# Optimization experiments

Hardware: AMD Instinct MI355X
Metric: run time of the kernel (lower is better)

## Reference

```python
import jax, jax.numpy as jnp
import numpy as np

DIM = 512
HEADS = 8
DIM_HEAD = 64
INNER = HEADS * DIM_HEAD  # 512
B, N = 4, 2048


def setup_inputs() -> dict:
    key = jax.random.key(0)
    k1, k2, k3, k4 = jax.random.split(key, 4)
    x = jax.random.normal(k1, (B, N, DIM), dtype=jnp.float32)
    # nn.Linear(dim, inner*3, bias=False): weight [3*inner, dim]; store transposed [dim, 3*inner]
    w_qkv = jax.random.normal(k2, (DIM, 3 * INNER), dtype=jnp.float32) / np.sqrt(DIM)
    w_out = jax.random.normal(k3, (INNER, DIM), dtype=jnp.float32) / np.sqrt(INNER)
    b_out = jax.random.normal(k4, (DIM,), dtype=jnp.float32) * 0.01
    return {"x": x, "w_qkv": w_qkv, "w_out": w_out, "b_out": b_out}


def reference(x, w_qkv, w_out, b_out):
    b, n, _ = x.shape
    scale = DIM_HEAD ** -0.5
    qkv = x @ w_qkv  # [b, n, 3*inner]
    q, k, v = jnp.split(qkv, 3, axis=-1)
    # [b, n, h, d] -> [b, h, n, d]
    reshape = lambda t: t.reshape(b, n, HEADS, DIM_HEAD).transpose(0, 2, 1, 3)
    q, k, v = reshape(q), reshape(k), reshape(v)
    dots = jnp.einsum('bhid,bhjd->bhij', q, k) * scale  # [b, h, n, n]
    attn = jax.nn.softmax(dots, axis=-1)
    out = jnp.einsum('bhij,bhjd->bhid', attn, v)  # [b, h, n, d]
    out = out.transpose(0, 2, 1, 3).reshape(b, n, INNER)
    return out @ w_out + b_out  # dropout is identity at inference
```

## Files before the change

### kernel.cpp

```cpp
#include <hip/hip_runtime.h>
#include <hip/hip_bf16.h>
#include <cstdint>

#define DEV __device__ __forceinline__

typedef __attribute__((ext_vector_type(8))) __bf16 bf16x8;
typedef __attribute__((ext_vector_type(4))) float floatx4;
typedef __attribute__((ext_vector_type(4))) short shortx4;
typedef __attribute__((ext_vector_type(8))) short shortx8;

constexpr float QSCALE = 0.18033688011112042f;

DEV unsigned short f2b(float f) {
  union { float f; unsigned u; } v; v.f = f;
  return (unsigned short)((v.u + 0x7fffu + ((v.u >> 16) & 1u)) >> 16);
}

#if defined(__has_builtin) && __has_builtin(__builtin_amdgcn_cvt_pk_bf16_f32)
DEV unsigned pk2(float a, float b) {
  typedef __attribute__((ext_vector_type(2))) __bf16 bf2;
  union { bf2 v; unsigned u; } u;
  u.v = __builtin_amdgcn_cvt_pk_bf16_f32(a, b);
  return u.u;
}
#else
DEV unsigned pk2(float a, float b) {
  return (unsigned)f2b(a) | ((unsigned)f2b(b) << 16);
}
#endif

#if defined(__has_builtin) && __has_builtin(__builtin_amdgcn_exp2f)
DEV float fexp2(float x) { return __builtin_amdgcn_exp2f(x); }
#else
DEV float fexp2(float x) { return exp2f(x); }
#endif

DEV floatx4 mfma16(bf16x8 a, bf16x8 b, floatx4 c) {
  return __builtin_amdgcn_mfma_f32_16x16x32_bf16(a, b, c, 0, 0, 0);
}

#define GLD_LDS16(gp, lp)                                                          \
  __builtin_amdgcn_global_load_lds(                                                \
      (const __attribute__((address_space(1))) void*)(gp),                         \
      (__attribute__((address_space(3))) void*)(lp), 16, 0, 0)

__global__ void prep(const float* __restrict__ x,
                     const float* __restrict__ w_qkv,
                     const float* __restrict__ w_out,
                     unsigned short* __restrict__ xb,
                     unsigned short* __restrict__ wqkvt,
                     unsigned short* __restrict__ woutt) {
  __shared__ float tile[32][33];
  if (blockIdx.x < 4096) {
    int i = blockIdx.x * 256 + threadIdx.x;
    floatx4 f = ((const floatx4*)x)[i];
    shortx4 s;
    s[0] = (short)f2b(f[0]); s[1] = (short)f2b(f[1]);
    s[2] = (short)f2b(f[2]); s[3] = (short)f2b(f[3]);
    ((shortx4*)xb)[i] = s;
    return;
  }
  int id = blockIdx.x - 4096;
  int bxr = id & 63, by = id >> 6;
  const float* in; unsigned short* out; int C, bx;
  if (bxr < 48) { in = w_qkv; out = wqkvt; C = 1536; bx = bxr; }
  else { in = w_out; out = woutt; C = 512; bx = bxr - 48; }
  const int R = 512;
  int tx = threadIdx.x & 31, ty = threadIdx.x >> 5;
  int r0 = by * 32, c0 = bx * 32;
#pragma unroll
  for (int i = 0; i < 4; i++) {
    int rr = ty + i * 8;
    tile[rr][tx] = in[(size_t)(r0 + rr) * C + c0 + tx];
  }
  __syncthreads();
#pragma unroll
  for (int i = 0; i < 4; i++) {
    int rr = ty + i * 8;
    out[(size_t)(c0 + rr) * R + r0 + tx] = f2b(tile[tx][rr]);
  }
}

__global__ __launch_bounds__(256, 3) void gemm_qkv(
    const unsigned short* __restrict__ A, const unsigned short* __restrict__ Bt,
    unsigned short* __restrict__ qf, unsigned short* __restrict__ kg,
    unsigned short* __restrict__ vf) {
  __shared__ __align__(16) unsigned short smem[17408];
  const int tid = threadIdx.x;
  const int lane = tid & 63, wid = tid >> 6;
  const int g = lane >> 4, r = lane & 15;
  const int flat = blockIdx.y * 12 + blockIdx.x;
  const int sw = (flat & 7) * 96 + (flat >> 3);
  const int bx = sw % 12, by = sw / 12;
  const int m0 = by * 128, n0 = bx * 128;
  const int wm = (wid & 1) * 64, wn = (wid >> 1) * 64;
  const int K = 512;

  floatx4 acc[4][4] = {};

  int rowA[2], kbA[2];
#pragma unroll
  for (int i = 0; i < 2; i++) {
    int c = i * 256 + tid;
    rowA[i] = c >> 2;
    kbA[i] = (c & 3) ^ ((rowA[i] >> 1) & 3);
  }

#define STAGE_G(kt, b)                                                           \
  {                                                                              \
    _Pragma("unroll") for (int i = 0; i < 2; i++) {                              \
      GLD_LDS16(A + (size_t)(m0 + rowA[i]) * K + (kt) + kbA[i] * 8,              \
                (char*)smem + (b)*8192 + i * 4096 + wid * 1024);                 \
      GLD_LDS16(Bt + (size_t)(n0 + rowA[i]) * K + (kt) + kbA[i] * 8,             \
                (char*)smem + 16384 + (b)*8192 + i * 4096 + wid * 1024);         \
    }                                                                            \
  }

  STAGE_G(0, 0)
  for (int it = 0; it < 16; it++) {
    const int buf = it & 1;
    __syncthreads();
    if (it + 1 < 16) STAGE_G((it + 1) * 32, buf ^ 1)
    const unsigned short* Xs = smem + buf * 4096;
    const unsigned short* Ws = smem + 8192 + buf * 4096;
    bf16x8 a[4], b[4];
#pragma unroll
    for (int t = 0; t < 4; t++) {
      int rw = wm + t * 16 + r;
      a[t] = *(const bf16x8*)(Xs + rw * 32 + (g ^ ((rw >> 1) & 3)) * 8);
      int rb = wn + t * 16 + r;
      b[t] = *(const bf16x8*)(Ws + rb * 32 + (g ^ ((rb >> 1) & 3)) * 8);
    }
#pragma unroll
    for (int mt = 0; mt < 4; mt++)
#pragma unroll
      for (int nt = 0; nt < 4; nt++)
        acc[mt][nt] = mfma16(a[mt], b[nt], acc[mt][nt]);
  }
#undef STAGE_G

  const int which = bx >> 2;
  if (which == 2) {
    const int tokbase = m0 + wm;
    const int bb = tokbase >> 11, vt = (tokbase & 2047) >> 6;
#pragma unroll
    for (int nt = 0; nt < 4; nt++) {
      int vcol = n0 + wn + nt * 16 + r - 1024;
      int h = vcol >> 6;
      size_t hb = (size_t)(bb * 8 + h) * 131072 + (size_t)vt * 4096 + nt * 1024 +
                  (g * 16 + r) * 8;
#pragma unroll
      for (int kc = 0; kc < 2; kc++) {
        union { unsigned u[4]; shortx8 v; } w;
        w.u[0] = pk2(acc[2 * kc][nt][0], acc[2 * kc][nt][1]);
        w.u[1] = pk2(acc[2 * kc][nt][2], acc[2 * kc][nt][3]);
        w.u[2] = pk2(acc[2 * kc + 1][nt][0], acc[2 * kc + 1][nt][1]);
        w.u[3] = pk2(acc[2 * kc + 1][nt][2], acc[2 * kc + 1][nt][3]);
        *(shortx8*)(vf + hb + kc * 512) = w.v;
      }
    }
  } else {
    const float sc = (which == 0) ? QSCALE : 1.f;
    __syncthreads();
#pragma unroll
    for (int mt = 0; mt < 4; mt++)
#pragma unroll
      for (int nt = 0; nt < 4; nt++) {
        int col = wn + nt * 16 + r;
#pragma unroll
        for (int e = 0; e < 4; e++)
          smem[(wm + mt * 16 + g * 4 + e) * 136 + col] = f2b(acc[mt][nt][e] * sc);
      }
    __syncthreads();
#pragma unroll
    for (int it = 0; it < 8; it++) {
      int c = it * 256 + tid;
      int row = c >> 4, cc = c & 15;
      shortx8 v = *(const shortx8*)(smem + row * 136 + cc * 8);
      int gq = n0 + cc * 8;
      int h = (gq >> 6) & 7, d0 = gq & 63;
      int tok = m0 + row, bb = tok >> 11, n = tok & 2047;
      if (which == 0) {
        int kc = d0 >> 5, gp = (d0 >> 3) & 3;
        *(shortx8*)(qf + (size_t)(bb * 8 + h) * 131072 + (n >> 4) * 1024 +
                    kc * 512 + (gp * 16 + (n & 15)) * 8) = v;
      } else {
        *(shortx8*)(kg + ((size_t)(bb * 8 + h) * 2048 + n) * 64 + d0) = v;
      }
    }
  }
}

__global__ __launch_bounds__(256, 2) void gemm_out(
    const unsigned short* __restrict__ A, const unsigned short* __restrict__ Bt,
    float* __restrict__ outF, const float* __restrict__ bias) {
  __shared__ __align__(16) unsigned short smem[16896];
  const int tid = threadIdx.x;
  const int lane = tid & 63, wid = tid >> 6;
  const int g = lane >> 4, r = lane & 15;
  const int m0 = blockIdx.y * 64, n0 = blockIdx.x * 128;
  const int wn = wid * 32;
  const int K = 512;

  floatx4 acc[4][2] = {};

  const int rA = tid >> 2, kA = (tid & 3) ^ ((rA >> 1) & 3);
  int rB[2], kB[2];
#pragma unroll
  for (int i = 0; i < 2; i++) {
    int c = i * 256 + tid;
    rB[i] = c >> 2;
    kB[i] = (c & 3) ^ ((rB[i] >> 1) & 3);
  }

#define STAGE_O(kt, b)                                                           \
  {                                                                              \
    GLD_LDS16(A + (size_t)(m0 + rA) * K + (kt) + kA * 8,                         \
              (char*)smem + (b)*4096 + wid * 1024);                              \
    _Pragma("unroll") for (int i = 0; i < 2; i++)                                \
        GLD_LDS16(Bt + (size_t)(n0 + rB[i]) * K + (kt) + kB[i] * 8,              \
                  (char*)smem + 8192 + (b)*8192 + i * 4096 + wid * 1024);        \
  }

  STAGE_O(0, 0)
  for (int it = 0; it < 16; it++) {
    const int buf = it & 1;
    __syncthreads();
    if (it + 1 < 16) STAGE_O((it + 1) * 32, buf ^ 1)
    const unsigned short* Xs = smem + buf * 2048;
    const unsigned short* Ws = smem + 4096 + buf * 4096;
    bf16x8 a[4], b[2];
#pragma unroll
    for (int t = 0; t < 4; t++) {
      int rw = t * 16 + r;
      a[t] = *(const bf16x8*)(Xs + rw * 32 + (g ^ ((rw >> 1) & 3)) * 8);
    }
#pragma unroll
    for (int t = 0; t < 2; t++) {
      int rb = wn + t * 16 + r;
      b[t] = *(const bf16x8*)(Ws + rb * 32 + (g ^ ((rb >> 1) & 3)) * 8);
    }
#pragma unroll
    for (int mt = 0; mt < 4; mt++)
#pragma unroll
      for (int bt = 0; bt < 2; bt++)
        acc[mt][bt] = mfma16(a[mt], b[bt], acc[mt][bt]);
  }
#undef STAGE_O

  float* ftile = (float*)smem;
  __syncthreads();
#pragma unroll
  for (int mt = 0; mt < 4; mt++)
#pragma unroll
    for (int bt = 0; bt < 2; bt++)
#pragma unroll
      for (int e = 0; e < 4; e++)
        ftile[(mt * 16 + g * 4 + e) * 132 + wn + bt * 16 + r] = acc[mt][bt][e];
  __syncthreads();
#pragma unroll
  for (int it = 0; it < 8; it++) {
    int c = it * 256 + tid;
    int lr = c >> 5, cc = c & 31;
    floatx4 v = *(const floatx4*)(ftile + lr * 132 + cc * 4);
    int col = n0 + cc * 4;
    v += *(const floatx4*)(bias + col);
    *(floatx4*)(outF + (size_t)(m0 + lr) * 512 + col) = v;
  }
}

__global__ __launch_bounds__(256, 2) void attn(
    const unsigned short* __restrict__ qf, const unsigned short* __restrict__ kg,
    const unsigned short* __restrict__ vf, unsigned short* __restrict__ ao) {
  __shared__ __align__(16) char L[65536];
  unsigned short* Ksm = (unsigned short*)L;
  const int tid = threadIdx.x, lane = tid & 63, wid = tid >> 6;
  const int g = lane >> 4, r = lane & 15, r7 = r & 7;
  const int wq = wid & 1, wk = wid >> 1;
  const int slot = blockIdx.x;
  const int bh = ((slot & 7) << 2) | ((slot >> 3) & 3);
  const int qt = slot >> 5;
  const size_t kbase = (size_t)bh * (2048 * 64);
  const size_t fbase = (size_t)bh * 131072;
  const int srow = lane >> 3;
  const int chunk = (lane & 7) ^ (srow & 7);

  const int qt0 = qt * 8 + wq * 4;
  bf16x8 bq[4][2];
#pragma unroll
  for (int nt = 0; nt < 4; nt++)
#pragma unroll
    for (int kc = 0; kc < 2; kc++)
      bq[nt][kc] = *(const bf16x8*)(qf + fbase + (size_t)(qt0 + nt) * 1024 +
                                    kc * 512 + lane * 8);

  bf16x8 vones;
#pragma unroll
  for (int i = 0; i < 8; i++) vones[i] = (__bf16)1.0f;
  const floatx4 fzero = {0.f, 0.f, 0.f, 0.f};

  floatx4 o[4][4] = {};
  floatx4 lacc[4] = {};

  const unsigned short* vbp = vf + fbase + (size_t)(wk * 2) * 4096 + lane * 8;
  const unsigned short* kgp =
      kg + kbase + (size_t)(wid * 64 + srow) * 64 + chunk * 8;

#define STAGE_K(b)                                                               \
  {                                                                              \
    _Pragma("unroll") for (int j = 0; j < 8; j++) {                              \
      GLD_LDS16(kgp + j * 512, (char*)L + (b)*32768 + wid * 8192 + j * 1024);    \
    }                                                                            \
    kgp += 16384;                                                                \
  }

  STAGE_K(0)
  for (int rnd = 0; rnd < 8; rnd++) {
    const int buf = rnd & 1;
    __syncthreads();
    if (rnd + 1 < 8) STAGE_K(buf ^ 1)
    const unsigned short* Kt = Ksm + buf * 16384 + wk * 8192;
#pragma unroll
    for (int sub = 0; sub < 2; sub++) {
      const unsigned short* Ks_ = Kt + sub * 4096;

      bf16x8 bv[4][2];
#pragma unroll
      for (int b = 0; b < 4; b++)
#pragma unroll
        for (int kc = 0; kc < 2; kc++)
          bv[b][kc] = *(const bf16x8*)(vbp + sub * 4096 + b * 1024 + kc * 512);

      floatx4 st[4][4];
      __builtin_amdgcn_s_setprio(1);
#pragma unroll
      for (int mt = 0; mt < 4; mt++) {
        bf16x8 ak0 = *(const bf16x8*)(Ks_ + (mt * 16 + r) * 64 + (g ^ r7) * 8);
        bf16x8 ak1 =
            *(const bf16x8*)(Ks_ + (mt * 16 + r) * 64 + ((4 + g) ^ r7) * 8);
#pragma unroll
        for (int nt = 0; nt < 4; nt++) {
          floatx4 t = mfma16(ak0, bq[nt][0], fzero);
          st[mt][nt] = mfma16(ak1, bq[nt][1], t);
        }
      }
      __builtin_amdgcn_s_setprio(0);

      bf16x8 ap[4][2];
#pragma unroll
      for (int a = 0; a < 4; a++) {
        float p[4][4];
#pragma unroll
        for (int mt = 0; mt < 4; mt++)
#pragma unroll
          for (int e = 0; e < 4; e++) p[mt][e] = fexp2(st[mt][a][e]);
#pragma unroll
        for (int kc = 0; kc < 2; kc++) {
          union { unsigned u[4]; bf16x8 v; } w;
          w.u[0] = pk2(p[2 * kc][0], p[2 * kc][1]);
          w.u[1] = pk2(p[2 * kc][2], p[2 * kc][3]);
          w.u[2] = pk2(p[2 * kc + 1][0], p[2 * kc + 1][1]);
          w.u[3] = pk2(p[2 * kc + 1][2], p[2 * kc + 1][3]);
          ap[a][kc] = w.v;
        }
      }

      __builtin_amdgcn_s_setprio(1);
#pragma unroll
      for (int kc = 0; kc < 2; kc++)
#pragma unroll
        for (int a = 0; a < 4; a++) {
          lacc[a] = mfma16(ap[a][kc], vones, lacc[a]);
#pragma unroll
          for (int b = 0; b < 4; b++)
            o[a][b] = mfma16(ap[a][kc], bv[b][kc], o[a][b]);
        }
      __builtin_amdgcn_s_setprio(0);
    }
    vbp += 16384;
  }
#undef STAGE_K

  float* fP = (float*)L;
  float* fL = (float*)(L + 32768);
  unsigned short* Osm = (unsigned short*)(L + 40960);
  __syncthreads();
  if (wk == 1) {
#pragma unroll
    for (int a = 0; a < 4; a++) {
      *(floatx4*)&fL[wq * 1024 + a * 256 + lane * 4] = lacc[a];
#pragma unroll
      for (int b = 0; b < 4; b++)
        *(floatx4*)&fP[wq * 4096 + (a * 4 + b) * 256 + lane * 4] = o[a][b];
    }
  }
  __syncthreads();
  if (wk == 0) {
#pragma unroll
    for (int a = 0; a < 4; a++) {
      floatx4 lt = lacc[a] + *(floatx4*)&fL[wq * 1024 + a * 256 + lane * 4];
      floatx4 il;
#pragma unroll
      for (int e = 0; e < 4; e++) il[e] = 1.f / lt[e];
#pragma unroll
      for (int b = 0; b < 4; b++) {
        floatx4 oo = o[a][b] +
                     *(floatx4*)&fP[wq * 4096 + (a * 4 + b) * 256 + lane * 4];
#pragma unroll
        for (int e = 0; e < 4; e++)
          Osm[wq * 4608 + (a * 16 + g * 4 + e) * 72 + b * 16 + r] =
              f2b(oo[e] * il[e]);
      }
    }
  }
  __syncthreads();
  const int bb = bh >> 3, h = bh & 7;
#pragma unroll
  for (int it = 0; it < 4; it++) {
    int c = it * 256 + tid;
    int row = c >> 3, cc = c & 7;
    int wqi = row >> 6, r6 = row & 63;
    shortx8 v = *(const shortx8*)(Osm + wqi * 4608 + r6 * 72 + cc * 8);
    int tok = qt * 128 + row;
    *(shortx8*)(ao + ((size_t)(bb * 2048 + tok)) * 512 + h * 64 + cc * 8) = v;
  }
}

extern "C" void kernel_launch(void* const* d_in, const int* in_sizes, int n_in,
                              void* d_out, int out_size, void* d_ws, size_t ws_size,
                              hipStream_t stream) {
  const float* x = (const float*)d_in[0];
  const float* w_qkv = (const float*)d_in[1];
  const float* w_out = (const float*)d_in[2];
  const float* b_out = (const float*)d_in[3];
  float* out = (float*)d_out;

  unsigned short* wsp = (unsigned short*)d_ws;
  unsigned short* xb = wsp;
  unsigned short* wqkvt = xb + (size_t)8192 * 512;
  unsigned short* woutt = wqkvt + (size_t)1536 * 512;
  unsigned short* qf = woutt + (size_t)512 * 512;
  unsigned short* kg = qf + (size_t)32 * 2048 * 64;
  unsigned short* vf = kg + (size_t)32 * 2048 * 64;
  unsigned short* ao = vf + (size_t)32 * 2048 * 64;

  prep<<<5120, 256, 0, stream>>>(x, w_qkv, w_out, xb, wqkvt, woutt);
  gemm_qkv<<<dim3(12, 64), 256, 0, stream>>>(xb, wqkvt, qf, kg, vf);
  attn<<<dim3(512), 256, 0, stream>>>(qf, kg, vf, ao);
  gemm_out<<<dim3(4, 128), 256, 0, stream>>>(ao, woutt, out, b_out);
}
```

Measured before the change: 147.9 us.

## Store Q row-major like K and use 2-wave 64x128 tiles in output GEMM

The QKV GEMM epilogue now writes Q in the same plain [bh, n, d] layout as K, replacing the fragment-packed layout, and the attention kernel loads Q fragments from that row-major buffer. The output GEMM switches from 4 waves of 64x32 tiles to 2 waves of 64x64 tiles per block (128 threads). Each wave therefore does more MFMAs per LDS fragment load. The epilogue is staged through a smaller shared tile in two passes. This trades fewer waves per block and extra barriers in the epilogue for better register reuse and lower shared-memory use.

```diff
diff --git a/kernel.cpp b/kernel.cpp
--- a/kernel.cpp
+++ b/kernel.cpp
@@ -83,7 +83,7 @@
 
 __global__ __launch_bounds__(256, 3) void gemm_qkv(
     const unsigned short* __restrict__ A, const unsigned short* __restrict__ Bt,
-    unsigned short* __restrict__ qf, unsigned short* __restrict__ kg,
+    unsigned short* __restrict__ qg, unsigned short* __restrict__ kg,
     unsigned short* __restrict__ vf) {
   __shared__ __align__(16) unsigned short smem[17408];
   const int tid = threadIdx.x;
@@ -161,6 +161,7 @@
     }
   } else {
     const float sc = (which == 0) ? QSCALE : 1.f;
+    unsigned short* dst = (which == 0) ? qg : kg;
     __syncthreads();
 #pragma unroll
     for (int mt = 0; mt < 4; mt++)
@@ -180,46 +181,47 @@
       int gq = n0 + cc * 8;
       int h = (gq >> 6) & 7, d0 = gq & 63;
       int tok = m0 + row, bb = tok >> 11, n = tok & 2047;
-      if (which == 0) {
-        int kc = d0 >> 5, gp = (d0 >> 3) & 3;
-        *(shortx8*)(qf + (size_t)(bb * 8 + h) * 131072 + (n >> 4) * 1024 +
-                    kc * 512 + (gp * 16 + (n & 15)) * 8) = v;
-      } else {
-        *(shortx8*)(kg + ((size_t)(bb * 8 + h) * 2048 + n) * 64 + d0) = v;
-      }
-    }
-  }
-}
-
-__global__ __launch_bounds__(256, 2) void gemm_out(
+      *(shortx8*)(dst + ((size_t)(bb * 8 + h) * 2048 + n) * 64 + d0) = v;
+    }
+  }
+}
+
+__global__ __launch_bounds__(128, 3) void gemm_out(
     const unsigned short* __restrict__ A, const unsigned short* __restrict__ Bt,
     float* __restrict__ outF, const float* __restrict__ bias) {
-  __shared__ __align__(16) unsigned short smem[16896];
+  __shared__ __align__(16) unsigned short smem[12288];
   const int tid = threadIdx.x;
   const int lane = tid & 63, wid = tid >> 6;
   const int g = lane >> 4, r = lane & 15;
   const int m0 = blockIdx.y * 64, n0 = blockIdx.x * 128;
-  const int wn = wid * 32;
+  const int wn = wid * 64;
   const int K = 512;
 
-  floatx4 acc[4][2] = {};
-
-  const int rA = tid >> 2, kA = (tid & 3) ^ ((rA >> 1) & 3);
-  int rB[2], kB[2];
+  floatx4 acc[4][4] = {};
+
+  int rowA[2], kA[2];
 #pragma unroll
   for (int i = 0; i < 2; i++) {
-    int c = i * 256 + tid;
-    rB[i] = c >> 2;
-    kB[i] = (c & 3) ^ ((rB[i] >> 1) & 3);
+    int c = i * 128 + tid;
+    rowA[i] = c >> 2;
+    kA[i] = (c & 3) ^ ((rowA[i] >> 1) & 3);
+  }
+  int rowB[4], kB[4];
+#pragma unroll
+  for (int i = 0; i < 4; i++) {
+    int c = i * 128 + tid;
+    rowB[i] = c >> 2;
+    kB[i] = (c & 3) ^ ((rowB[i] >> 1) & 3);
   }
 
 #define STAGE_O(kt, b)                                                           \
   {                                                                              \
-    GLD_LDS16(A + (size_t)(m0 + rA) * K + (kt) + kA * 8,                         \
-              (char*)smem + (b)*4096 + wid * 1024);                              \
     _Pragma("unroll") for (int i = 0; i < 2; i++)                                \
-        GLD_LDS16(Bt + (size_t)(n0 + rB[i]) * K + (kt) + kB[i] * 8,              \
-                  (char*)smem + 8192 + (b)*8192 + i * 4096 + wid * 1024);        \
+        GLD_LDS16(A + (size_t)(m0 + rowA[i]) * K + (kt) + kA[i] * 8,             \
+                  (char*)smem + (b)*4096 + i * 2048 + wid * 1024);               \
+    _Pragma("unroll") for (int i = 0; i < 4; i++)                                \
+        GLD_LDS16(Bt + (size_t)(n0 + rowB[i]) * K + (kt) + kB[i] * 8,            \
+                  (char*)smem + 8192 + (b)*8192 + i * 2048 + wid * 1024);        \
   }
 
   STAGE_O(0, 0)
@@ -229,48 +231,51 @@
     if (it + 1 < 16) STAGE_O((it + 1) * 32, buf ^ 1)
     const unsigned short* Xs = smem + buf * 2048;
     const unsigned short* Ws = smem + 4096 + buf * 4096;
-    bf16x8 a[4], b[2];
+    bf16x8 a[4], b[4];
 #pragma unroll
     for (int t = 0; t < 4; t++) {
       int rw = t * 16 + r;
       a[t] = *(const bf16x8*)(Xs + rw * 32 + (g ^ ((rw >> 1) & 3)) * 8);
-    }
-#pragma unroll
-    for (int t = 0; t < 2; t++) {
       int rb = wn + t * 16 + r;
       b[t] = *(const bf16x8*)(Ws + rb * 32 + (g ^ ((rb >> 1) & 3)) * 8);
     }
 #pragma unroll
     for (int mt = 0; mt < 4; mt++)
 #pragma unroll
-      for (int bt = 0; bt < 2; bt++)
-        acc[mt][bt] = mfma16(a[mt], b[bt], acc[mt][bt]);
+      for (int nt = 0; nt < 4; nt++)
+        acc[mt][nt] = mfma16(a[mt], b[nt], acc[mt][nt]);
   }
 #undef STAGE_O
 
   float* ftile = (float*)smem;
   __syncthreads();
 #pragma unroll
-  for (int mt = 0; mt < 4; mt++)
-#pragma unroll
-    for (int bt = 0; bt < 2; bt++)
-#pragma unroll
-      for (int e = 0; e < 4; e++)
-        ftile[(mt * 16 + g * 4 + e) * 132 + wn + bt * 16 + r] = acc[mt][bt][e];
-  __syncthreads();
-#pragma unroll
-  for (int it = 0; it < 8; it++) {
-    int c = it * 256 + tid;
-    int lr = c >> 5, cc = c & 31;
-    floatx4 v = *(const floatx4*)(ftile + lr * 132 + cc * 4);
-    int col = n0 + cc * 4;
-    v += *(const floatx4*)(bias + col);
-    *(floatx4*)(outF + (size_t)(m0 + lr) * 512 + col) = v;
+  for (int pass = 0; pass < 2; pass++) {
+    if (wid == pass) {
+#pragma unroll
+      for (int mt = 0; mt < 4; mt++)
+#pragma unroll
+        for (int nt = 0; nt < 4; nt++)
+#pragma unroll
+          for (int e = 0; e < 4; e++)
+            ftile[(mt * 16 + g * 4 + e) * 68 + nt * 16 + r] = acc[mt][nt][e];
+    }
+    __syncthreads();
+#pragma unroll
+    for (int it = 0; it < 8; it++) {
+      int c = it * 128 + tid;
+      int lr = c >> 4, cc = c & 15;
+      floatx4 v = *(const floatx4*)(ftile + lr * 68 + cc * 4);
+      int col = n0 + pass * 64 + cc * 4;
+      v += *(const floatx4*)(bias + col);
+      *(floatx4*)(outF + (size_t)(m0 + lr) * 512 + col) = v;
+    }
+    __syncthreads();
   }
 }
 
 __global__ __launch_bounds__(256, 2) void attn(
-    const unsigned short* __restrict__ qf, const unsigned short* __restrict__ kg,
+    const unsigned short* __restrict__ qg, const unsigned short* __restrict__ kg,
     const unsigned short* __restrict__ vf, unsigned short* __restrict__ ao) {
   __shared__ __align__(16) char L[65536];
   unsigned short* Ksm = (unsigned short*)L;
@@ -285,14 +290,14 @@
   const int srow = lane >> 3;
   const int chunk = (lane & 7) ^ (srow & 7);
 
-  const int qt0 = qt * 8 + wq * 4;
+  const unsigned short* qgp =
+      qg + kbase + (size_t)(qt * 128 + wq * 64 + r) * 64;
   bf16x8 bq[4][2];
 #pragma unroll
   for (int nt = 0; nt < 4; nt++)
 #pragma unroll
     for (int kc = 0; kc < 2; kc++)
-      bq[nt][kc] = *(const bf16x8*)(qf + fbase + (size_t)(qt0 + nt) * 1024 +
-                                    kc * 512 + lane * 8);
+      bq[nt][kc] = *(const bf16x8*)(qgp + nt * 1024 + kc * 32 + g * 8);
 
   bf16x8 vones;
 #pragma unroll
@@ -439,13 +444,13 @@
   unsigned short* xb = wsp;
   unsigned short* wqkvt = xb + (size_t)8192 * 512;
   unsigned short* woutt = wqkvt + (size_t)1536 * 512;
-  unsigned short* qf = woutt + (size_t)512 * 512;
-  unsigned short* kg = qf + (size_t)32 * 2048 * 64;
+  unsigned short* qg = woutt + (size_t)512 * 512;
+  unsigned short* kg = qg + (size_t)32 * 2048 * 64;
   unsigned short* vf = kg + (size_t)32 * 2048 * 64;
   unsigned short* ao = vf + (size_t)32 * 2048 * 64;
 
   prep<<<5120, 256, 0, stream>>>(x, w_qkv, w_out, xb, wqkvt, woutt);
-  gemm_qkv<<<dim3(12, 64), 256, 0, stream>>>(xb, wqkvt, qf, kg, vf);
-  attn<<<dim3(512), 256, 0, stream>>>(qf, kg, vf, ao);
-  gemm_out<<<dim3(4, 128), 256, 0, stream>>>(ao, woutt, out, b_out);
-}
+  gemm_qkv<<<dim3(12, 64), 256, 0, stream>>>(xb, wqkvt, qg, kg, vf);
+  attn<<<dim3(512), 256, 0, stream>>>(qg, kg, vf, ao);
+  gemm_out<<<dim3(4, 128), 128, 0, stream>>>(ao, woutt, out, b_out);
+}
```

Result: no change. 148.2 us (+0.2%).
